# Optimization experiments

Measured on AMD Instinct MI355X. Metric: run time of the kernel, lower is better.

Reference implementation:

```python
import jax, jax.numpy as jnp
import numpy as np

C = 512
C8 = C // 8   # query/key dim = 64
C2 = C // 2   # value dim = 256


def setup_inputs() -> dict:
    key = jax.random.key(0)
    ks = jax.random.split(key, 10)
    B, H, W = 4, 64, 64
    x = jax.random.normal(ks[0], (B, H, W, C), dtype=jnp.float32)
    # 1x1 conv kernels expressed as [in_ch, out_ch] matrices + biases
    Wf = jax.random.normal(ks[1], (C, C8), dtype=jnp.float32) * 0.02
    bf = jnp.zeros((C8,), dtype=jnp.float32)
    Wg = jax.random.normal(ks[2], (C, C8), dtype=jnp.float32) * 0.02
    bg = jnp.zeros((C8,), dtype=jnp.float32)
    Wh = jax.random.normal(ks[3], (C, C2), dtype=jnp.float32) * 0.02
    bh = jnp.zeros((C2,), dtype=jnp.float32)
    Wo = jax.random.normal(ks[4], (C2, C), dtype=jnp.float32) * 0.02
    bo = jnp.zeros((C,), dtype=jnp.float32)
    gamma = jax.random.normal(ks[5], (1,), dtype=jnp.float32) * 0.05
    return {"x": x, "Wf": Wf, "bf": bf, "Wg": Wg, "bg": bg,
            "Wh": Wh, "bh": bh, "Wo": Wo, "bo": bo, "gamma": gamma}


def reference(x, Wf, bf, Wg, bg, Wh, bh, Wo, bo, gamma):
    B, H, W, _ = x.shape
    N = H * W
    xf = x.reshape(B, N, C)                               # flatten spatial dims
    f = xf @ Wf + bf                                      # [B, N, C8] keys
    g = xf @ Wg + bg                                      # [B, N, C8] queries
    h = xf @ Wh + bh                                      # [B, N, C2] values
    s = jnp.einsum('bnd,bmd->bnm', g, f)                  # [B, N, N] scores (g @ f^T)
    beta = jax.nn.softmax(s, axis=-1)                     # attention map
    o = jnp.einsum('bnm,bmd->bnd', beta, h)               # [B, N, C2]
    o = o @ Wo + bo                                       # [B, N, C] output 1x1 conv
    out = gamma * o + xf                                  # residual with learned scale
    return out.reshape(B, H, W, C)
```

## Files before the change

### kernel.cpp

```cpp
#include <hip/hip_runtime.h>
#include <math.h>

#define B_   4
#define N_   4096
#define C_   512
#define C8_  64
#define C2_  256
#define LOG2E 1.4426950408889634f

typedef __attribute__((ext_vector_type(8))) short bf16x8;
typedef __attribute__((ext_vector_type(4))) short bf16x4;
typedef __attribute__((ext_vector_type(4))) float floatx4;
typedef __attribute__((ext_vector_type(16))) float floatx16;
typedef __attribute__((ext_vector_type(2))) unsigned uint32x2;

__device__ __forceinline__ short f2bf(float x) {
    unsigned u = __float_as_uint(x);
    u += 0x7fff + ((u >> 16) & 1);
    return (short)(u >> 16);
}
__device__ __forceinline__ unsigned cvtpk(float a, float b) {
    unsigned r;
    asm("v_cvt_pk_bf16_f32 %0, %1, %2" : "=v"(r) : "v"(a), "v"(b));
    return r;
}

union U8 { bf16x8 v; unsigned u[4]; };
union U4 { bf16x4 v; unsigned u[2]; };

__global__ __launch_bounds__(256) void convert_all(
    const float* __restrict__ x,
    const float* __restrict__ Wf, const float* __restrict__ Wg,
    const float* __restrict__ Wh, const float* __restrict__ Wo,
    short* __restrict__ WcatT, short* __restrict__ WoT,
    short* __restrict__ xbf)
{
    const int NX = (B_ * N_ * C_) / 4;
    int tid = blockIdx.x * 256 + threadIdx.x;
    if (tid < NX) {
        float4 v = ((const float4*)x)[tid];
        U4 pk; pk.u[0] = cvtpk(v.x, v.y); pk.u[1] = cvtpk(v.z, v.w);
        ((bf16x4*)xbf)[tid] = pk.v;
    } else {
        int t1 = tid - NX;
        if (t1 < 384 * 512) {
            int n = t1 >> 9, k = t1 & 511;
            float v = (n < 64)  ? Wf[k * 64 + n]
                    : (n < 128) ? Wg[k * 64 + (n - 64)]
                                : Wh[k * 256 + (n - 128)];
            WcatT[t1] = f2bf(v);
        } else {
            int t2 = t1 - 384 * 512;
            int n = t2 >> 8, k = t2 & 255;
            WoT[t2] = f2bf(Wo[k * 512 + n]);
        }
    }
}

__global__ __launch_bounds__(256, 2) void qkv_mfma(
    const short* __restrict__ xbf, const short* __restrict__ WcatT,
    const float* __restrict__ bfv, const float* __restrict__ bgv,
    const float* __restrict__ bhv,
    short* __restrict__ fbf, short* __restrict__ gbf, short* __restrict__ hT)
{
    const int ny = blockIdx.x;
    const int m0 = blockIdx.y * 128;
    const int n0 = ny * 128;
    const int t  = threadIdx.x;
    const int w  = t >> 6, lane = t & 63;
    const int l15 = lane & 15, quad = lane >> 4;
    const int wm = w & 1, wn = w >> 1;

    __shared__ short As[128 * 40];
    __shared__ short Bs[128 * 40];

    floatx4 acc[4][4];
    #pragma unroll
    for (int i = 0; i < 4; i++)
        #pragma unroll
        for (int j = 0; j < 4; j++) acc[i][j] = (floatx4){0.f,0.f,0.f,0.f};

    for (int k0 = 0; k0 < C_; k0 += 32) {
        #pragma unroll
        for (int i = 0; i < 2; i++) {
            int c = t + i * 256;
            int row = c >> 2, ko = (c & 3) * 8;
            *(bf16x8*)&As[row * 40 + ko] =
                *(const bf16x8*)&xbf[(size_t)(m0 + row) * C_ + k0 + ko];
        }
        #pragma unroll
        for (int i = 0; i < 2; i++) {
            int c = t + i * 256;
            int nr = c >> 2, ko = (c & 3) * 8;
            *(bf16x8*)&Bs[nr * 40 + ko] =
                *(const bf16x8*)&WcatT[(size_t)(n0 + nr) * 512 + k0 + ko];
        }
        __syncthreads();

        bf16x8 af[4], bfr[4];
        #pragma unroll
        for (int mt = 0; mt < 4; mt++)
            af[mt] = *(const bf16x8*)&As[(wm * 64 + mt * 16 + l15) * 40 + quad * 8];
        #pragma unroll
        for (int nt = 0; nt < 4; nt++)
            bfr[nt] = *(const bf16x8*)&Bs[(wn * 64 + nt * 16 + l15) * 40 + quad * 8];
        #pragma unroll
        for (int mt = 0; mt < 4; mt++)
            #pragma unroll
            for (int nt = 0; nt < 4; nt++)
                acc[mt][nt] = __builtin_amdgcn_mfma_f32_16x16x32_bf16(af[mt], bfr[nt], acc[mt][nt], 0, 0, 0);
        __syncthreads();
    }

    if (ny == 0) {
        #pragma unroll
        for (int mt = 0; mt < 4; mt++) {
            #pragma unroll
            for (int nt = 0; nt < 4; nt++) {
                int cn = wn * 64 + nt * 16 + l15;
                #pragma unroll
                for (int rg = 0; rg < 4; rg++) {
                    int row = m0 + wm * 64 + mt * 16 + quad * 4 + rg;
                    float v = acc[mt][nt][rg];
                    if (cn < 64) fbf[(size_t)row * 64 + cn]        = f2bf(v + bfv[cn]);
                    else         gbf[(size_t)row * 64 + (cn - 64)] = f2bf((v + bgv[cn - 64]) * LOG2E);
                }
            }
        }
    } else {
        #pragma unroll
        for (int mt = 0; mt < 4; mt++) {
            #pragma unroll
            for (int nt = 0; nt < 4; nt++) {
                int hch = (ny - 1) * 128 + wn * 64 + nt * 16 + l15;
                int row = m0 + wm * 64 + mt * 16 + quad * 4;
                int bb = row >> 12, n = row & 4095;
                float bias = bhv[hch];
                U4 pk;
                pk.u[0] = cvtpk(acc[mt][nt][0] + bias, acc[mt][nt][1] + bias);
                pk.u[1] = cvtpk(acc[mt][nt][2] + bias, acc[mt][nt][3] + bias);
                *(bf16x4*)&hT[((size_t)(bb * 256 + hch)) * 4096 + n] = pk.v;
            }
        }
    }
}

#define HST 40

__global__ __launch_bounds__(256, 2) void attn_v6(
    const short* __restrict__ fK,
    const short* __restrict__ gQ,
    const short* __restrict__ hT,
    float* __restrict__ oPart,
    float* __restrict__ lPart,
    int sbits)
{
    const int bx = blockIdx.x;
    const int s  = bx & ((1 << sbits) - 1);
    const int vh = (bx >> sbits) & 1;
    const int qt = (bx >> (sbits + 1)) & 31;
    const int b  = bx >> (sbits + 6);
    const int kb = s << (12 - sbits);
    const int niter = 64 >> sbits;
    const int t  = threadIdx.x;
    const int w  = t >> 6, lane = t & 63;
    const int l31 = lane & 31, h = lane >> 5;
    const int q_wave = qt * 128 + w * 32;

    __shared__ short fs[2][64 * HST];
    __shared__ short hs[2][128 * HST];

    bf16x8 qf[4];
    #pragma unroll
    for (int k = 0; k < 4; k++)
        qf[k] = *(const bf16x8*)&gQ[(size_t)(b * N_ + q_wave + l31) * 64 + k * 16 + h * 8];

    floatx16 oacc[4];
    #pragma unroll
    for (int vt = 0; vt < 4; vt++)
        #pragma unroll
        for (int j = 0; j < 16; j++) oacc[vt][j] = 0.f;
    float lsum = 0.f;

    const int f_row = t >> 2, f_c = (t & 3) * 16;
    const int h_row = t >> 3, h_c = (t & 7) * 8;

    {
        *(bf16x8*)&fs[0][f_row * HST + f_c] =
            *(const bf16x8*)&fK[(size_t)(b * N_ + kb + f_row) * 64 + f_c];
        *(bf16x8*)&fs[0][f_row * HST + f_c + 8] =
            *(const bf16x8*)&fK[(size_t)(b * N_ + kb + f_row) * 64 + f_c + 8];
        #pragma unroll
        for (int i = 0; i < 4; i++)
            *(bf16x8*)&hs[0][(h_row + i * 32) * HST + h_c] =
                *(const bf16x8*)&hT[((size_t)(b * 256 + vh * 128 + h_row + i * 32)) * 4096 + kb + h_c];
    }
    __syncthreads();

    for (int it = 0; it < niter; ++it) {
        const int cur = it & 1;
        const bool more = (it < niter - 1);
        const int kn = kb + (it + 1) * 64;

        bf16x8 rf0, rf1, rh[4];
        if (more) {
            rf0 = *(const bf16x8*)&fK[(size_t)(b * N_ + kn + f_row) * 64 + f_c];
            rf1 = *(const bf16x8*)&fK[(size_t)(b * N_ + kn + f_row) * 64 + f_c + 8];
            #pragma unroll
            for (int i = 0; i < 4; i++)
                rh[i] = *(const bf16x8*)&hT[((size_t)(b * 256 + vh * 128 + h_row + i * 32)) * 4096 + kn + h_c];
        }

        bf16x8 ffr[2][4];
        #pragma unroll
        for (int m = 0; m < 2; m++)
            #pragma unroll
            for (int k = 0; k < 4; k++)
                ffr[m][k] = *(const bf16x8*)&fs[cur][(m * 32 + l31) * HST + k * 16 + h * 8];

        floatx16 sacc[2];
        __builtin_amdgcn_s_setprio(1);
        #pragma unroll
        for (int m = 0; m < 2; m++) {
            #pragma unroll
            for (int j = 0; j < 16; j++) sacc[m][j] = 0.f;
            #pragma unroll
            for (int k = 0; k < 4; k++)
                sacc[m] = __builtin_amdgcn_mfma_f32_32x32x16_bf16(
                    ffr[m][k], qf[k], sacc[m], 0, 0, 0);
        }
        __builtin_amdgcn_s_setprio(0);

        bf16x8 pfrag[4];
        #pragma unroll
        for (int m = 0; m < 2; m++) {
            float p[16]; float ps_ = 0.f;
            #pragma unroll
            for (int j = 0; j < 16; j++) {
                p[j] = __builtin_amdgcn_exp2f(sacc[m][j]);
                ps_ += p[j];
            }
            ps_ += __shfl_xor(ps_, 32);
            lsum += ps_;
            unsigned pk[8];
            #pragma unroll
            for (int i = 0; i < 8; i++) pk[i] = cvtpk(p[2 * i], p[2 * i + 1]);
            #pragma unroll
            for (int kp = 0; kp < 2; kp++) {
                uint32x2 r0 = __builtin_amdgcn_permlane32_swap(pk[4 * kp],     pk[4 * kp + 2], false, false);
                uint32x2 r1 = __builtin_amdgcn_permlane32_swap(pk[4 * kp + 1], pk[4 * kp + 3], false, false);
                U8 u; u.u[0] = r0[0]; u.u[1] = r1[0]; u.u[2] = r0[1]; u.u[3] = r1[1];
                pfrag[m * 2 + kp] = u.v;
            }
        }

        __builtin_amdgcn_s_setprio(1);
        #pragma unroll
        for (int kk = 0; kk < 4; kk++)
            #pragma unroll
            for (int vt = 0; vt < 4; vt++) {
                bf16x8 vfr = *(const bf16x8*)&hs[cur][(vt * 32 + l31) * HST + kk * 16 + h * 8];
                oacc[vt] = __builtin_amdgcn_mfma_f32_32x32x16_bf16(
                    pfrag[kk], vfr, oacc[vt], 0, 0, 0);
            }
        __builtin_amdgcn_s_setprio(0);

        if (more) {
            const int nxt = cur ^ 1;
            *(bf16x8*)&fs[nxt][f_row * HST + f_c] = rf0;
            *(bf16x8*)&fs[nxt][f_row * HST + f_c + 8] = rf1;
            #pragma unroll
            for (int i = 0; i < 4; i++)
                *(bf16x8*)&hs[nxt][(h_row + i * 32) * HST + h_c] = rh[i];
        }
        __syncthreads();
    }

    #pragma unroll
    for (int vt = 0; vt < 4; vt++) {
        int vch = vh * 128 + vt * 32 + l31;
        #pragma unroll
        for (int r = 0; r < 16; r++) {
            int q = q_wave + (r & 3) + 8 * (r >> 2) + 4 * h;
            oPart[(size_t)s * 4194304 + (size_t)(b * N_ + q) * 256 + vch] = oacc[vt][r];
        }
    }
    if (vh == 0 && lane < 32)
        lPart[(size_t)s * 16384 + b * N_ + q_wave + lane] = lsum;
}

__global__ __launch_bounds__(256) void attn_combine(
    const float* __restrict__ oPart, const float* __restrict__ lPart,
    short* __restrict__ obf, int nsplit)
{
    int idx = blockIdx.x * 256 + threadIdx.x;
    int row = idx >> 6;
    int c4  = (idx & 63) << 2;
    float4 a = *(const float4*)&oPart[(size_t)row * 256 + c4];
    float l = lPart[row];
    for (int s2 = 1; s2 < nsplit; s2++) {
        float4 bv = *(const float4*)&oPart[(size_t)s2 * 4194304 + (size_t)row * 256 + c4];
        a.x += bv.x; a.y += bv.y; a.z += bv.z; a.w += bv.w;
        l += lPart[(size_t)s2 * 16384 + row];
    }
    float inv = 1.0f / l;
    U4 o;
    o.u[0] = cvtpk(a.x * inv, a.y * inv);
    o.u[1] = cvtpk(a.z * inv, a.w * inv);
    *(bf16x4*)&obf[(size_t)row * 256 + c4] = o.v;
}

__global__ __launch_bounds__(256, 2) void out_mfma(
    const short* __restrict__ obf, const short* __restrict__ WoT,
    const float* __restrict__ bo, const float* __restrict__ x,
    const float* __restrict__ gamma, float* __restrict__ out)
{
    const int n0 = blockIdx.x * 128;
    const int m0 = blockIdx.y * 128;
    const int t  = threadIdx.x;
    const int w  = t >> 6, lane = t & 63;
    const int l15 = lane & 15, quad = lane >> 4;
    const int wm = w & 1, wn = w >> 1;

    __shared__ short As[128 * 40];
    __shared__ short Bs[128 * 40];

    floatx4 acc[4][4];
    #pragma unroll
    for (int i = 0; i < 4; i++)
        #pragma unroll
        for (int j = 0; j < 4; j++) acc[i][j] = (floatx4){0.f,0.f,0.f,0.f};

    for (int k0 = 0; k0 < C2_; k0 += 32) {
        #pragma unroll
        for (int i = 0; i < 2; i++) {
            int c = t + i * 256;
            int row = c >> 2, ko = (c & 3) * 8;
            *(bf16x8*)&As[row * 40 + ko] =
                *(const bf16x8*)&obf[(size_t)(m0 + row) * 256 + k0 + ko];
        }
        #pragma unroll
        for (int i = 0; i < 2; i++) {
            int c = t + i * 256;
            int nr = c >> 2, ko = (c & 3) * 8;
            *(bf16x8*)&Bs[nr * 40 + ko] =
                *(const bf16x8*)&WoT[(size_t)(n0 + nr) * 256 + k0 + ko];
        }
        __syncthreads();

        bf16x8 af[4], bfr[4];
        #pragma unroll
        for (int mt = 0; mt < 4; mt++)
            af[mt] = *(const bf16x8*)&As[(wm * 64 + mt * 16 + l15) * 40 + quad * 8];
        #pragma unroll
        for (int nt = 0; nt < 4; nt++)
            bfr[nt] = *(const bf16x8*)&Bs[(wn * 64 + nt * 16 + l15) * 40 + quad * 8];
        #pragma unroll
        for (int mt = 0; mt < 4; mt++)
            #pragma unroll
            for (int nt = 0; nt < 4; nt++)
                acc[mt][nt] = __builtin_amdgcn_mfma_f32_16x16x32_bf16(af[mt], bfr[nt], acc[mt][nt], 0, 0, 0);
        __syncthreads();
    }

    const float gm = gamma[0];
    #pragma unroll
    for (int mt = 0; mt < 4; mt++) {
        #pragma unroll
        for (int nt = 0; nt < 4; nt++) {
            int col = n0 + wn * 64 + nt * 16 + l15;
            float bias = bo[col];
            #pragma unroll
            for (int rg = 0; rg < 4; rg++) {
                int row = m0 + wm * 64 + mt * 16 + quad * 4 + rg;
                out[(size_t)row * C_ + col] =
                    gm * (acc[mt][nt][rg] + bias) + x[(size_t)row * C_ + col];
            }
        }
    }
}

extern "C" void kernel_launch(void* const* d_in, const int* in_sizes, int n_in,
                              void* d_out, int out_size, void* d_ws, size_t ws_size,
                              hipStream_t stream) {
    (void)in_sizes; (void)n_in; (void)out_size; (void)ws_size;

    const float* x     = (const float*)d_in[0];
    const float* Wf    = (const float*)d_in[1];
    const float* bfv   = (const float*)d_in[2];
    const float* Wg    = (const float*)d_in[3];
    const float* bgv   = (const float*)d_in[4];
    const float* Wh    = (const float*)d_in[5];
    const float* bhv   = (const float*)d_in[6];
    const float* Wo    = (const float*)d_in[7];
    const float* bo    = (const float*)d_in[8];
    const float* gamma = (const float*)d_in[9];
    float* out = (float*)d_out;

    short* fbf   = (short*)d_ws;
    short* gbf   = fbf   + (size_t)B_ * N_ * C8_;
    short* hT    = gbf   + (size_t)B_ * N_ * C8_;
    short* obf   = hT    + (size_t)B_ * C2_ * N_;
    short* WcatT = obf   + (size_t)B_ * N_ * C2_;
    short* WoT   = WcatT + (size_t)384 * 512;
    short* xbf   = WoT   + (size_t)512 * 256;
    float* oPart = (float*)(xbf + (size_t)B_ * N_ * C_);
    float* lPart = oPart + (size_t)2 * 16384 * 256;

    const int sbits = 1;

    convert_all<<<9472, 256, 0, stream>>>(x, Wf, Wg, Wh, Wo, WcatT, WoT, xbf);
    qkv_mfma<<<dim3(3, 128), 256, 0, stream>>>(xbf, WcatT, bfv, bgv, bhv, fbf, gbf, hT);
    attn_v6<<<256 << sbits, 256, 0, stream>>>(fbf, gbf, hT, oPart, lPart, sbits);
    attn_combine<<<4096, 256, 0, stream>>>(oPart, lPart, obf, 1 << sbits);
    out_mfma<<<dim3(4, 128), 256, 0, stream>>>(obf, WoT, bo, x, gamma, out);
}
```

Baseline: 208.6 us.

## Fuse split-K combine into output GEMM, store partials as bf16, retile QKV

Removes the separate attn_combine kernel. The output projection now loads both bf16 attention partials, adds them, scales by the inverse row sums and converts while staging the A tile. The partial outputs are stored as bf16 instead of fp32, which halves partial traffic but adds rounding before the combine. The QKV GEMM tile drops to 64 rows so the grid has more blocks, and the output GEMM moves to 64x256 tiles.

```diff
diff --git a/kernel.cpp b/kernel.cpp
--- a/kernel.cpp
+++ b/kernel.cpp
@@ -23,6 +23,9 @@
     unsigned r;
     asm("v_cvt_pk_bf16_f32 %0, %1, %2" : "=v"(r) : "v"(a), "v"(b));
     return r;
+}
+__device__ __forceinline__ float bf2f(short s) {
+    return __uint_as_float(((unsigned)(unsigned short)s) << 16);
 }
 
 union U8 { bf16x8 v; unsigned u[4]; };
@@ -57,34 +60,32 @@
     }
 }
 
-__global__ __launch_bounds__(256, 2) void qkv_mfma(
+__global__ __launch_bounds__(256, 3) void qkv_mfma(
     const short* __restrict__ xbf, const short* __restrict__ WcatT,
     const float* __restrict__ bfv, const float* __restrict__ bgv,
     const float* __restrict__ bhv,
     short* __restrict__ fbf, short* __restrict__ gbf, short* __restrict__ hT)
 {
     const int ny = blockIdx.x;
-    const int m0 = blockIdx.y * 128;
+    const int m0 = blockIdx.y * 64;
     const int n0 = ny * 128;
     const int t  = threadIdx.x;
     const int w  = t >> 6, lane = t & 63;
     const int l15 = lane & 15, quad = lane >> 4;
     const int wm = w & 1, wn = w >> 1;
 
-    __shared__ short As[128 * 40];
+    __shared__ short As[64 * 40];
     __shared__ short Bs[128 * 40];
 
-    floatx4 acc[4][4];
-    #pragma unroll
-    for (int i = 0; i < 4; i++)
+    floatx4 acc[2][4];
+    #pragma unroll
+    for (int i = 0; i < 2; i++)
         #pragma unroll
         for (int j = 0; j < 4; j++) acc[i][j] = (floatx4){0.f,0.f,0.f,0.f};
 
     for (int k0 = 0; k0 < C_; k0 += 32) {
-        #pragma unroll
-        for (int i = 0; i < 2; i++) {
-            int c = t + i * 256;
-            int row = c >> 2, ko = (c & 3) * 8;
+        {
+            int row = t >> 2, ko = (t & 3) * 8;
             *(bf16x8*)&As[row * 40 + ko] =
                 *(const bf16x8*)&xbf[(size_t)(m0 + row) * C_ + k0 + ko];
         }
@@ -97,15 +98,15 @@
         }
         __syncthreads();
 
-        bf16x8 af[4], bfr[4];
-        #pragma unroll
-        for (int mt = 0; mt < 4; mt++)
-            af[mt] = *(const bf16x8*)&As[(wm * 64 + mt * 16 + l15) * 40 + quad * 8];
+        bf16x8 af[2], bfr[4];
+        #pragma unroll
+        for (int mt = 0; mt < 2; mt++)
+            af[mt] = *(const bf16x8*)&As[(wm * 32 + mt * 16 + l15) * 40 + quad * 8];
         #pragma unroll
         for (int nt = 0; nt < 4; nt++)
             bfr[nt] = *(const bf16x8*)&Bs[(wn * 64 + nt * 16 + l15) * 40 + quad * 8];
         #pragma unroll
-        for (int mt = 0; mt < 4; mt++)
+        for (int mt = 0; mt < 2; mt++)
             #pragma unroll
             for (int nt = 0; nt < 4; nt++)
                 acc[mt][nt] = __builtin_amdgcn_mfma_f32_16x16x32_bf16(af[mt], bfr[nt], acc[mt][nt], 0, 0, 0);
@@ -114,13 +115,13 @@
 
     if (ny == 0) {
         #pragma unroll
-        for (int mt = 0; mt < 4; mt++) {
+        for (int mt = 0; mt < 2; mt++) {
             #pragma unroll
             for (int nt = 0; nt < 4; nt++) {
                 int cn = wn * 64 + nt * 16 + l15;
                 #pragma unroll
                 for (int rg = 0; rg < 4; rg++) {
-                    int row = m0 + wm * 64 + mt * 16 + quad * 4 + rg;
+                    int row = m0 + wm * 32 + mt * 16 + quad * 4 + rg;
                     float v = acc[mt][nt][rg];
                     if (cn < 64) fbf[(size_t)row * 64 + cn]        = f2bf(v + bfv[cn]);
                     else         gbf[(size_t)row * 64 + (cn - 64)] = f2bf((v + bgv[cn - 64]) * LOG2E);
@@ -129,11 +130,11 @@
         }
     } else {
         #pragma unroll
-        for (int mt = 0; mt < 4; mt++) {
+        for (int mt = 0; mt < 2; mt++) {
             #pragma unroll
             for (int nt = 0; nt < 4; nt++) {
                 int hch = (ny - 1) * 128 + wn * 64 + nt * 16 + l15;
-                int row = m0 + wm * 64 + mt * 16 + quad * 4;
+                int row = m0 + wm * 32 + mt * 16 + quad * 4;
                 int bb = row >> 12, n = row & 4095;
                 float bias = bhv[hch];
                 U4 pk;
@@ -151,7 +152,7 @@
     const short* __restrict__ fK,
     const short* __restrict__ gQ,
     const short* __restrict__ hT,
-    float* __restrict__ oPart,
+    short* __restrict__ oPart,
     float* __restrict__ lPart,
     int sbits)
 {
@@ -282,65 +283,58 @@
         #pragma unroll
         for (int r = 0; r < 16; r++) {
             int q = q_wave + (r & 3) + 8 * (r >> 2) + 4 * h;
-            oPart[(size_t)s * 4194304 + (size_t)(b * N_ + q) * 256 + vch] = oacc[vt][r];
+            oPart[(size_t)s * 4194304 + (size_t)(b * N_ + q) * 256 + vch] = f2bf(oacc[vt][r]);
         }
     }
     if (vh == 0 && lane < 32)
         lPart[(size_t)s * 16384 + b * N_ + q_wave + lane] = lsum;
 }
 
-__global__ __launch_bounds__(256) void attn_combine(
-    const float* __restrict__ oPart, const float* __restrict__ lPart,
-    short* __restrict__ obf, int nsplit)
-{
-    int idx = blockIdx.x * 256 + threadIdx.x;
-    int row = idx >> 6;
-    int c4  = (idx & 63) << 2;
-    float4 a = *(const float4*)&oPart[(size_t)row * 256 + c4];
-    float l = lPart[row];
-    for (int s2 = 1; s2 < nsplit; s2++) {
-        float4 bv = *(const float4*)&oPart[(size_t)s2 * 4194304 + (size_t)row * 256 + c4];
-        a.x += bv.x; a.y += bv.y; a.z += bv.z; a.w += bv.w;
-        l += lPart[(size_t)s2 * 16384 + row];
-    }
-    float inv = 1.0f / l;
-    U4 o;
-    o.u[0] = cvtpk(a.x * inv, a.y * inv);
-    o.u[1] = cvtpk(a.z * inv, a.w * inv);
-    *(bf16x4*)&obf[(size_t)row * 256 + c4] = o.v;
-}
-
 __global__ __launch_bounds__(256, 2) void out_mfma(
-    const short* __restrict__ obf, const short* __restrict__ WoT,
+    const short* __restrict__ oPart, const float* __restrict__ lPart,
+    const short* __restrict__ WoT,
     const float* __restrict__ bo, const float* __restrict__ x,
     const float* __restrict__ gamma, float* __restrict__ out)
 {
-    const int n0 = blockIdx.x * 128;
-    const int m0 = blockIdx.y * 128;
+    const int n0 = blockIdx.x * 256;
+    const int m0 = blockIdx.y * 64;
     const int t  = threadIdx.x;
     const int w  = t >> 6, lane = t & 63;
     const int l15 = lane & 15, quad = lane >> 4;
     const int wm = w & 1, wn = w >> 1;
 
-    __shared__ short As[128 * 40];
-    __shared__ short Bs[128 * 40];
-
-    floatx4 acc[4][4];
-    #pragma unroll
-    for (int i = 0; i < 4; i++)
-        #pragma unroll
-        for (int j = 0; j < 4; j++) acc[i][j] = (floatx4){0.f,0.f,0.f,0.f};
+    __shared__ short As[64 * 40];
+    __shared__ short Bs[256 * 40];
+    __shared__ float linv[64];
+
+    if (t < 64)
+        linv[t] = 1.0f / (lPart[m0 + t] + lPart[16384 + m0 + t]);
+    __syncthreads();
+
+    floatx4 acc[2][8];
+    #pragma unroll
+    for (int i = 0; i < 2; i++)
+        #pragma unroll
+        for (int j = 0; j < 8; j++) acc[i][j] = (floatx4){0.f,0.f,0.f,0.f};
 
     for (int k0 = 0; k0 < C2_; k0 += 32) {
-        #pragma unroll
-        for (int i = 0; i < 2; i++) {
-            int c = t + i * 256;
-            int row = c >> 2, ko = (c & 3) * 8;
-            *(bf16x8*)&As[row * 40 + ko] =
-                *(const bf16x8*)&obf[(size_t)(m0 + row) * 256 + k0 + ko];
-        }
-        #pragma unroll
-        for (int i = 0; i < 2; i++) {
+        {
+            int row = t >> 2, ko = (t & 3) * 8;
+            size_t gb = (size_t)(m0 + row) * 256 + k0 + ko;
+            bf16x8 o0 = *(const bf16x8*)&oPart[gb];
+            bf16x8 o1 = *(const bf16x8*)&oPart[4194304 + gb];
+            float li = linv[row];
+            U8 u;
+            #pragma unroll
+            for (int j = 0; j < 4; j++) {
+                float a0 = (bf2f(o0[2 * j])     + bf2f(o1[2 * j]))     * li;
+                float a1 = (bf2f(o0[2 * j + 1]) + bf2f(o1[2 * j + 1])) * li;
+                u.u[j] = cvtpk(a0, a1);
+            }
+            *(bf16x8*)&As[row * 40 + ko] = u.v;
+        }
+        #pragma unroll
+        for (int i = 0; i < 4; i++) {
             int c = t + i * 256;
             int nr = c >> 2, ko = (c & 3) * 8;
             *(bf16x8*)&Bs[nr * 40 + ko] =
@@ -348,31 +342,31 @@
         }
         __syncthreads();
 
-        bf16x8 af[4], bfr[4];
-        #pragma unroll
-        for (int mt = 0; mt < 4; mt++)
-            af[mt] = *(const bf16x8*)&As[(wm * 64 + mt * 16 + l15) * 40 + quad * 8];
-        #pragma unroll
-        for (int nt = 0; nt < 4; nt++)
-            bfr[nt] = *(const bf16x8*)&Bs[(wn * 64 + nt * 16 + l15) * 40 + quad * 8];
-        #pragma unroll
-        for (int mt = 0; mt < 4; mt++)
-            #pragma unroll
-            for (int nt = 0; nt < 4; nt++)
+        bf16x8 af[2], bfr[8];
+        #pragma unroll
+        for (int mt = 0; mt < 2; mt++)
+            af[mt] = *(const bf16x8*)&As[(wm * 32 + mt * 16 + l15) * 40 + quad * 8];
+        #pragma unroll
+        for (int nt = 0; nt < 8; nt++)
+            bfr[nt] = *(const bf16x8*)&Bs[(wn * 128 + nt * 16 + l15) * 40 + quad * 8];
+        #pragma unroll
+        for (int mt = 0; mt < 2; mt++)
+            #pragma unroll
+            for (int nt = 0; nt < 8; nt++)
                 acc[mt][nt] = __builtin_amdgcn_mfma_f32_16x16x32_bf16(af[mt], bfr[nt], acc[mt][nt], 0, 0, 0);
         __syncthreads();
     }
 
     const float gm = gamma[0];
     #pragma unroll
-    for (int mt = 0; mt < 4; mt++) {
-        #pragma unroll
-        for (int nt = 0; nt < 4; nt++) {
-            int col = n0 + wn * 64 + nt * 16 + l15;
+    for (int mt = 0; mt < 2; mt++) {
+        #pragma unroll
+        for (int nt = 0; nt < 8; nt++) {
+            int col = n0 + wn * 128 + nt * 16 + l15;
             float bias = bo[col];
             #pragma unroll
             for (int rg = 0; rg < 4; rg++) {
-                int row = m0 + wm * 64 + mt * 16 + quad * 4 + rg;
+                int row = m0 + wm * 32 + mt * 16 + quad * 4 + rg;
                 out[(size_t)row * C_ + col] =
                     gm * (acc[mt][nt][rg] + bias) + x[(size_t)row * C_ + col];
             }
@@ -400,18 +394,16 @@
     short* fbf   = (short*)d_ws;
     short* gbf   = fbf   + (size_t)B_ * N_ * C8_;
     short* hT    = gbf   + (size_t)B_ * N_ * C8_;
-    short* obf   = hT    + (size_t)B_ * C2_ * N_;
-    short* WcatT = obf   + (size_t)B_ * N_ * C2_;
+    short* WcatT = hT    + (size_t)B_ * C2_ * N_;
     short* WoT   = WcatT + (size_t)384 * 512;
     short* xbf   = WoT   + (size_t)512 * 256;
-    float* oPart = (float*)(xbf + (size_t)B_ * N_ * C_);
-    float* lPart = oPart + (size_t)2 * 16384 * 256;
+    short* oPart = xbf   + (size_t)B_ * N_ * C_;
+    float* lPart = (float*)(oPart + (size_t)2 * 16384 * 256);
 
     const int sbits = 1;
 
     convert_all<<<9472, 256, 0, stream>>>(x, Wf, Wg, Wh, Wo, WcatT, WoT, xbf);
-    qkv_mfma<<<dim3(3, 128), 256, 0, stream>>>(xbf, WcatT, bfv, bgv, bhv, fbf, gbf, hT);
+    qkv_mfma<<<dim3(3, 256), 256, 0, stream>>>(xbf, WcatT, bfv, bgv, bhv, fbf, gbf, hT);
     attn_v6<<<256 << sbits, 256, 0, stream>>>(fbf, gbf, hT, oPart, lPart, sbits);
-    attn_combine<<<4096, 256, 0, stream>>>(oPart, lPart, obf, 1 << sbits);
-    out_mfma<<<dim3(4, 128), 256, 0, stream>>>(obf, WoT, bo, x, gamma, out);
-}
+    out_mfma<<<dim3(2, 256), 256, 0, stream>>>(oPart, lPart, WoT, bo, x, gamma, out);
+}
```

Result: faster. 195.6 us (-6.3%).
